# Performance work log

Measured on AMD Instinct MI355X. Metric: run time of the kernel, lower is better.

## Reference

```python
import jax, jax.numpy as jnp
import numpy as np

K = 3
TAPS = K * K
STD = float(np.sqrt(2.0)) / K  # FilterNorm scale: relu gain / kernel_size


def filter_norm(f, axis):
    # torch FilterNorm: subtract mean, divide by unbiased std (+1e-10), scale by STD
    m = jnp.mean(f, axis=axis, keepdims=True)
    sd = jnp.std(f, axis=axis, keepdims=True, ddof=1)
    return (f - m) / (sd + 1e-10) * STD


def setup_inputs() -> dict:
    key = jax.random.key(0)
    ks = jax.random.split(key, 9)
    B, C, H, W = 4, 64, 192, 192
    mid = int(C * 0.2)  # se_ratio=0.2 -> 12
    f = lambda k, shape, s: jax.random.normal(k, shape, jnp.float32) * s
    return {
        'x':   f(ks[0], (B, C, H, W), 1.0),
        'sw':  f(ks[1], (TAPS, C), 0.05),        # spatial branch 1x1 conv weight
        'sb':  f(ks[2], (TAPS,), 0.05),
        'cw1': f(ks[3], (mid, C), 0.05),         # channel branch squeeze
        'cb1': f(ks[4], (mid,), 0.05),
        'cw2': f(ks[5], (C * TAPS, mid), 0.05),  # channel branch expand
        'cb2': f(ks[6], (C * TAPS,), 0.05),
        'w2':  f(ks[7], (C, C, 1, 9), 0.05),     # trailing 1x9 conv
        'b2':  f(ks[8], (C,), 0.05),
    }


def block_forward(x, sw, sb, cw1, cb1, cw2, cb2, w2, b2):
    B, C, H, W = x.shape
    # --- DDFPack ---
    # spatial filters: 1x1 conv -> (B, 9, H, W), FilterNorm across the 9 taps
    s = jnp.einsum('bchw,tc->bthw', x, sw) + sb[None, :, None, None]
    s = filter_norm(s, axis=1)
    # channel filters: GAP -> 1x1 -> relu -> 1x1 -> (B, C, 9), FilterNorm over taps
    g = x.mean(axis=(2, 3))                         # (B, C)
    h1 = jax.nn.relu(g @ cw1.T + cb1)               # (B, mid)
    cf = (h1 @ cw2.T + cb2).reshape(B, C, TAPS)     # (B, C, 9)
    cf = filter_norm(cf, axis=2)
    # decoupled dynamic filter apply: per-pixel depthwise 3x3, combine='mul', pad=1
    xp = jnp.pad(x, ((0, 0), (0, 0), (1, 1), (1, 1)))
    out = jnp.zeros_like(x)
    for idx in range(TAPS):  # fixed 9-tap loop, no big unfold intermediate
        i, j = idx // K, idx % K
        out = out + xp[:, :, i:i + H, j:j + W] * s[:, idx:idx + 1] * cf[:, :, idx, None, None]
    # --- LeakyReLU(0.1) -> 1x9 conv (pad (0,4)) -> residual add (res_scale=1) ---
    a = jnp.where(out >= 0, out, 0.1 * out)
    y = jax.lax.conv_general_dilated(a, w2, (1, 1), ((0, 0), (4, 4)),
                                     dimension_numbers=('NCHW', 'OIHW', 'NCHW'))
    y = y + b2[None, :, None, None]
    return x + y


def reference(x, sw, sb, cw1, cb1, cw2, cb2, w2, b2):
    return block_forward(x, sw, sb, cw1, cb1, cw2, cb2, w2, b2)
```

## Files before the change

### kernel.cpp

```cpp
#include <hip/hip_runtime.h>
#include <hip/hip_bf16.h>

#define B_    4
#define C_    64
#define H_    192
#define W_    192
#define TAPS_ 9
#define MID_  12
#define HW_   (H_ * W_)
#define K_TOT 576
#define AT_STRIDE 72

constexpr float STD_ = 0.47140452079103173f;

using bf16 = __hip_bfloat16;
typedef __attribute__((ext_vector_type(4))) float  f32x4;
typedef __attribute__((ext_vector_type(8))) short  short8;

__device__ __forceinline__ unsigned short f2bf_bits(float v) {
    union { bf16 h; unsigned short u; } cv;
    cv.h = __float2bfloat16(v);
    return cv.u;
}

__device__ __forceinline__ int at_word(int row, int cw) {
    int key = (row >> 2) & 7;
    return row * (AT_STRIDE / 2) + ((((cw >> 2) ^ key) & 7) << 2) + (cw & 3);
}

__global__ __launch_bounds__(256) void k_pre(const float* __restrict__ x,
                                             const float* __restrict__ w2,
                                             unsigned short* __restrict__ w2bf,
                                             float* __restrict__ partials) {
    int bx = blockIdx.x;
    if (bx < 144) {
        int d = bx * 256 + threadIdx.x;
        int o = d / K_TOT;
        int rem = d - o * K_TOT;
        int t = rem >> 6;
        int c = rem & 63;
        w2bf[d] = f2bf_bits(w2[(o * C_ + c) * TAPS_ + t]);
        return;
    }
    bx -= 144;
    int bc = bx / 3, part = bx - 3 * (bx / 3);
    const float4* p = (const float4*)(x + (size_t)bc * HW_ + part * 12288);
    float s = 0.f;
    #pragma unroll
    for (int k = 0; k < 12; ++k) {
        float4 u = p[threadIdx.x + k * 256];
        s += u.x + u.y + u.z + u.w;
    }
    #pragma unroll
    for (int off = 32; off; off >>= 1) s += __shfl_down(s, off);
    __shared__ float red[4];
    if ((threadIdx.x & 63) == 0) red[threadIdx.x >> 6] = s;
    __syncthreads();
    if (threadIdx.x == 0)
        partials[bx] = red[0] + red[1] + red[2] + red[3];
}

__global__ __launch_bounds__(256, 3) void k_main(const float* __restrict__ x,
                                                 const float* __restrict__ sw,
                                                 const float* __restrict__ sb,
                                                 const float* __restrict__ partials,
                                                 const float* __restrict__ cw1,
                                                 const float* __restrict__ cb1,
                                                 const float* __restrict__ cw2,
                                                 const float* __restrict__ cb2,
                                                 const unsigned short* __restrict__ w2bf,
                                                 const float* __restrict__ bias2,
                                                 float* __restrict__ out) {
    __shared__ __align__(16) char smem[38624];
    short*          aT    = (short*)smem;
    unsigned*       aT32  = (unsigned*)smem;
    float*          sw_l  = (float*)smem;
    float*          s_l   = (float*)(smem + 28800);
    float*          b2_l  = (float*)(smem + 35712);
    float*          sb_l  = (float*)(smem + 35968);
    float*          cfn_l = (float*)(smem + 36016);
    float*          h1_l  = (float*)(smem + 38320);
    float*          g_l   = (float*)(smem + 38368);

    int bx = blockIdx.x;
    int bh = (bx & 7) * 96 + (bx >> 3);
    int bb = bh / H_;
    int h  = bh - bb * H_;
    int tid = threadIdx.x;
    int lane = tid & 63, wid = tid >> 6;
    int quad = lane >> 4, l16 = lane & 15;
    int obase = wid * 16;

    for (int i = tid; i < TAPS_ * C_; i += 256) sw_l[i] = sw[i];
    if (tid < C_) b2_l[tid] = bias2[tid];
    if (tid < TAPS_) sb_l[tid] = sb[tid];
    __syncthreads();

    const short* w2s = (const short*)w2bf;
    const short* arow = w2s + (obase + l16) * K_TOT + quad * 8;
    short8 a0 = *(const short8*)(arow);
    short8 a1 = *(const short8*)(arow + 32);

    if (tid < W_) {
        int w = tid;
        float acc[TAPS_];
        #pragma unroll
        for (int t = 0; t < TAPS_; ++t) acc[t] = sb_l[t];
        const float* px = x + (size_t)bb * C_ * HW_ + h * W_ + w;
        #pragma unroll 16
        for (int c = 0; c < C_; ++c) {
            float xv = px[(size_t)c * HW_];
            #pragma unroll
            for (int t = 0; t < TAPS_; ++t) acc[t] = fmaf(xv, sw_l[t * C_ + c], acc[t]);
        }
        float mean = 0.f;
        #pragma unroll
        for (int t = 0; t < TAPS_; ++t) mean += acc[t];
        mean *= (1.f / TAPS_);
        float var = 0.f;
        #pragma unroll
        for (int t = 0; t < TAPS_; ++t) { float d = acc[t] - mean; var += d * d; }
        var *= (1.f / (TAPS_ - 1));
        float scale = STD_ / (sqrtf(fmaxf(var, 0.f)) + 1e-10f);
        float* sp = s_l + (w & 3) * 432 + (w >> 2);
        #pragma unroll
        for (int t = 0; t < TAPS_; ++t) sp[t * 48] = (acc[t] - mean) * scale;
    } else {
        int c = lane;
        const float* pp = partials + (bb * C_ + c) * 3;
        g_l[c] = (pp[0] + pp[1] + pp[2]) * (1.0f / HW_);
        if (c < MID_) {
            float acc = cb1[c];
            #pragma unroll 8
            for (int cc = 0; cc < C_; ++cc) acc += g_l[cc] * cw1[c * C_ + cc];
            h1_l[c] = fmaxf(acc, 0.f);
        }
        float f[TAPS_];
        float mean = 0.f;
        #pragma unroll
        for (int t = 0; t < TAPS_; ++t) {
            int n = c * TAPS_ + t;
            float acc = cb2[n];
            #pragma unroll
            for (int m = 0; m < MID_; ++m) acc += h1_l[m] * cw2[n * MID_ + m];
            f[t] = acc;
            mean += acc;
        }
        mean *= (1.f / TAPS_);
        float var = 0.f;
        #pragma unroll
        for (int t = 0; t < TAPS_; ++t) { float d = f[t] - mean; var += d * d; }
        var *= (1.f / (TAPS_ - 1));
        float scale = STD_ / (sqrtf(fmaxf(var, 0.f)) + 1e-10f);
        #pragma unroll
        for (int t = 0; t < TAPS_; ++t)
            cfn_l[c * TAPS_ + t] = (f[t] - mean) * scale;
    }
    __syncthreads();

    for (int i = tid; i < 8 * (AT_STRIDE / 2); i += 256) {
        int rowIdx = i / (AT_STRIDE / 2);
        int col    = i - rowIdx * (AT_STRIDE / 2);
        int r = (rowIdx < 4) ? rowIdx : (192 + rowIdx);
        aT32[r * (AT_STRIDE / 2) + col] = 0u;
    }

    {
        int wbase = wid * 16;
        if (lane < 48) {
            int w0 = 4 * lane;
            float sreg[4][TAPS_];
            #pragma unroll
            for (int k = 0; k < 4; ++k) {
                const float* sp = s_l + k * 432 + lane;
                #pragma unroll
                for (int t = 0; t < TAPS_; ++t) sreg[k][t] = sp[t * 48];
            }
            bool l0 = (lane == 0), l47 = (lane == 47);
            int rok0 = (h > 0), rok2 = (h < H_ - 1);
            const float* xbase = x + (long)bb * C_ * HW_ + (long)(h - 1) * W_;
            #pragma unroll 2
            for (int i = 0; i < 16; i += 2) {
                int c0 = wbase + i;
                int cu = __builtin_amdgcn_readfirstlane(c0);
                const float* cfp = cfn_l + cu * TAPS_;
                const float* pc0 = xbase + (long)c0 * HW_;
                const float* pc1 = pc0 + HW_;
                float acc0[4] = {0.f, 0.f, 0.f, 0.f};
                float acc1[4] = {0.f, 0.f, 0.f, 0.f};
                #pragma unroll
                for (int r = 0; r < 3; ++r) {
                    if (r == 0 && !rok0) continue;
                    if (r == 2 && !rok2) continue;
                    const float* p0 = pc0 + r * W_;
                    const float* p1 = pc1 + r * W_;
                    float4 fa = *(const float4*)(p0 + w0);
                    float4 fb = *(const float4*)(p1 + w0);
                    float ma = __shfl_up(fa.w, 1);   ma = l0  ? 0.f : ma;
                    float mb = __shfl_up(fb.w, 1);   mb = l0  ? 0.f : mb;
                    float pa = __shfl_down(fa.x, 1); pa = l47 ? 0.f : pa;
                    float pb = __shfl_down(fb.x, 1); pb = l47 ? 0.f : pb;
                    float va[6] = { ma, fa.x, fa.y, fa.z, fa.w, pa };
                    float vb[6] = { mb, fb.x, fb.y, fb.z, fb.w, pb };
                    #pragma unroll
                    for (int dc = 0; dc < 3; ++dc) {
                        int t = r * 3 + dc;
                        float cva = cfp[t];
                        float cvb = cfp[TAPS_ + t];
                        #pragma unroll
                        for (int k = 0; k < 4; ++k) {
                            acc0[k] = fmaf(va[k + dc] * sreg[k][t], cva, acc0[k]);
                            acc1[k] = fmaf(vb[k + dc] * sreg[k][t], cvb, acc1[k]);
                        }
                    }
                }
                int cw = c0 >> 1;
                #pragma unroll
                for (int k = 0; k < 4; ++k) {
                    float a0v = acc0[k]; a0v = (a0v >= 0.f) ? a0v : 0.1f * a0v;
                    float a1v = acc1[k]; a1v = (a1v >= 0.f) ? a1v : 0.1f * a1v;
                    unsigned pk = (unsigned)f2bf_bits(a0v)
                                | ((unsigned)f2bf_bits(a1v) << 16);
                    aT32[at_word(w0 + k + 4, cw)] = pk;
                }
            }
        }
    }
    __syncthreads();

    {
        f32x4 acc[12];
        #pragma unroll
        for (int n = 0; n < 12; ++n) acc[n] = (f32x4){0.f, 0.f, 0.f, 0.f};

        #pragma unroll 1
        for (int kk = 0; kk < 18; ++kk) {
            short8 a2 = a1;
            if (kk < 16) a2 = *(const short8*)(arow + (kk + 2) * 32);
            int t = kk >> 1;
            int ch = ((kk & 1) << 2) + quad;
            int rowb = l16 + t;
            int key0 = (rowb >> 2) & 7;
            int off0 = rowb * AT_STRIDE + (((ch ^ key0) & 7) << 3);
            int off1 = rowb * AT_STRIDE + (((ch ^ key0 ^ 4) & 7) << 3);
            #pragma unroll
            for (int n = 0; n < 12; ++n) {
                int off = ((n & 1) ? off1 : off0) + n * 16 * AT_STRIDE;
                short8 bf = *(const short8*)(aT + off);
                acc[n] = __builtin_amdgcn_mfma_f32_16x16x32_bf16(a0, bf, acc[n], 0, 0, 0);
            }
            a0 = a1; a1 = a2;
        }

        size_t xbase = (size_t)bb * C_ * HW_ + (size_t)h * W_;
        #pragma unroll
        for (int n = 0; n < 12; ++n) {
            int w = n * 16 + l16;
            #pragma unroll
            for (int reg = 0; reg < 4; ++reg) {
                int o = obase + quad * 4 + reg;
                size_t idx = xbase + (size_t)o * HW_ + w;
                out[idx] = acc[n][reg] + b2_l[o] + x[idx];
            }
        }
    }
}

extern "C" void kernel_launch(void* const* d_in, const int* in_sizes, int n_in,
                              void* d_out, int out_size, void* d_ws, size_t ws_size,
                              hipStream_t stream) {
    const float* x   = (const float*)d_in[0];
    const float* sw  = (const float*)d_in[1];
    const float* sb  = (const float*)d_in[2];
    const float* cw1 = (const float*)d_in[3];
    const float* cb1 = (const float*)d_in[4];
    const float* cw2 = (const float*)d_in[5];
    const float* cb2 = (const float*)d_in[6];
    const float* w2  = (const float*)d_in[7];
    const float* b2  = (const float*)d_in[8];
    float* out = (float*)d_out;

    unsigned short* w2bf = (unsigned short*)d_ws;
    float* partials = (float*)((char*)d_ws + 73728);

    hipLaunchKernelGGL(k_pre, dim3(912), dim3(256), 0, stream, x, w2, w2bf, partials);
    hipLaunchKernelGGL(k_main, dim3(B_ * H_), dim3(256), 0, stream,
                       x, sw, sb, partials, cw1, cb1, cw2, cb2, w2bf, b2, out);
}
```

Before: 145.4 us.

## Prefetch input rows and batch channel loads to hide global memory latency

The spatial-filter 1x1 conv now issues its channel loads in batches of 16 into registers, with sched_barriers separating load and FMA groups, so many loads are in flight before the math starts. The dynamic-filter apply loop now software-pipelines its three input rows per channel pair: the first pair is loaded before the spatial phase and the next pair is prefetched during each iteration. Boundary rows are clamped and then zeroed by multiplying with a flag instead of branching. This aims to overlap global memory latency with compute, at the cost of higher register pressure and possible occupancy loss.

```diff
diff --git a/kernel.cpp b/kernel.cpp
--- a/kernel.cpp
+++ b/kernel.cpp
@@ -90,6 +90,7 @@
     int lane = tid & 63, wid = tid >> 6;
     int quad = lane >> 4, l16 = lane & 15;
     int obase = wid * 16;
+    int w0 = 4 * lane;
 
     for (int i = tid; i < TAPS_ * C_; i += 256) sw_l[i] = sw[i];
     if (tid < C_) b2_l[tid] = bias2[tid];
@@ -101,18 +102,61 @@
     short8 a0 = *(const short8*)(arow);
     short8 a1 = *(const short8*)(arow + 32);
 
+    long ro0 = (long)((h > 0) ? (h - 1) : h) * W_;
+    long ro1 = (long)h * W_;
+    long ro2 = (long)((h < H_ - 1) ? (h + 1) : h) * W_;
+    const float* xc = x + (size_t)bb * C_ * HW_;
+
+    float4 P0a, P1a, P2a, P0b, P1b, P2b;
+    if (lane < 48) {
+        const float* q0 = xc + (size_t)(wid * 16) * HW_;
+        const float* q1 = q0 + HW_;
+        P0a = *(const float4*)(q0 + ro0 + w0);
+        P1a = *(const float4*)(q0 + ro1 + w0);
+        P2a = *(const float4*)(q0 + ro2 + w0);
+        P0b = *(const float4*)(q1 + ro0 + w0);
+        P1b = *(const float4*)(q1 + ro1 + w0);
+        P2b = *(const float4*)(q1 + ro2 + w0);
+    }
+
     if (tid < W_) {
         int w = tid;
         float acc[TAPS_];
         #pragma unroll
         for (int t = 0; t < TAPS_; ++t) acc[t] = sb_l[t];
         const float* px = x + (size_t)bb * C_ * HW_ + h * W_ + w;
-        #pragma unroll 16
-        for (int c = 0; c < C_; ++c) {
-            float xv = px[(size_t)c * HW_];
-            #pragma unroll
-            for (int t = 0; t < TAPS_; ++t) acc[t] = fmaf(xv, sw_l[t * C_ + c], acc[t]);
-        }
+        float xv0[16], xv1[16];
+        #pragma unroll
+        for (int j = 0; j < 16; ++j) xv0[j] = px[(size_t)j * HW_];
+        #pragma unroll
+        for (int j = 0; j < 16; ++j) xv1[j] = px[(size_t)(16 + j) * HW_];
+        __builtin_amdgcn_sched_barrier(0);
+        #pragma unroll
+        for (int j = 0; j < 16; ++j)
+            #pragma unroll
+            for (int t = 0; t < TAPS_; ++t)
+                acc[t] = fmaf(xv0[j], sw_l[t * C_ + j], acc[t]);
+        #pragma unroll
+        for (int j = 0; j < 16; ++j) xv0[j] = px[(size_t)(32 + j) * HW_];
+        __builtin_amdgcn_sched_barrier(0);
+        #pragma unroll
+        for (int j = 0; j < 16; ++j)
+            #pragma unroll
+            for (int t = 0; t < TAPS_; ++t)
+                acc[t] = fmaf(xv1[j], sw_l[t * C_ + 16 + j], acc[t]);
+        #pragma unroll
+        for (int j = 0; j < 16; ++j) xv1[j] = px[(size_t)(48 + j) * HW_];
+        __builtin_amdgcn_sched_barrier(0);
+        #pragma unroll
+        for (int j = 0; j < 16; ++j)
+            #pragma unroll
+            for (int t = 0; t < TAPS_; ++t)
+                acc[t] = fmaf(xv0[j], sw_l[t * C_ + 32 + j], acc[t]);
+        #pragma unroll
+        for (int j = 0; j < 16; ++j)
+            #pragma unroll
+            for (int t = 0; t < TAPS_; ++t)
+                acc[t] = fmaf(xv1[j], sw_l[t * C_ + 48 + j], acc[t]);
         float mean = 0.f;
         #pragma unroll
         for (int t = 0; t < TAPS_; ++t) mean += acc[t];
@@ -166,9 +210,7 @@
     }
 
     {
-        int wbase = wid * 16;
         if (lane < 48) {
-            int w0 = 4 * lane;
             float sreg[4][TAPS_];
             #pragma unroll
             for (int k = 0; k < 4; ++k) {
@@ -177,43 +219,57 @@
                 for (int t = 0; t < TAPS_; ++t) sreg[k][t] = sp[t * 48];
             }
             bool l0 = (lane == 0), l47 = (lane == 47);
-            int rok0 = (h > 0), rok2 = (h < H_ - 1);
-            const float* xbase = x + (long)bb * C_ * HW_ + (long)(h - 1) * W_;
-            #pragma unroll 2
+            float rok0f = (h > 0)      ? 1.f : 0.f;
+            float rok2f = (h < H_ - 1) ? 1.f : 0.f;
+
+#define TAPROW(RR, FA, FB)                                                     \
+            do {                                                               \
+                float ma = __shfl_up(FA.w, 1);   ma = l0  ? 0.f : ma;          \
+                float mb = __shfl_up(FB.w, 1);   mb = l0  ? 0.f : mb;          \
+                float pa = __shfl_down(FA.x, 1); pa = l47 ? 0.f : pa;          \
+                float pb = __shfl_down(FB.x, 1); pb = l47 ? 0.f : pb;          \
+                float va[6] = { ma, FA.x, FA.y, FA.z, FA.w, pa };              \
+                float vb[6] = { mb, FB.x, FB.y, FB.z, FB.w, pb };              \
+                _Pragma("unroll")                                              \
+                for (int dc = 0; dc < 3; ++dc) {                               \
+                    int t = (RR) * 3 + dc;                                     \
+                    float cva = cfp[t];                                        \
+                    float cvb = cfp[TAPS_ + t];                                \
+                    _Pragma("unroll")                                          \
+                    for (int k = 0; k < 4; ++k) {                              \
+                        acc0[k] = fmaf(va[k + dc] * sreg[k][t], cva, acc0[k]); \
+                        acc1[k] = fmaf(vb[k + dc] * sreg[k][t], cvb, acc1[k]); \
+                    }                                                          \
+                }                                                              \
+            } while (0)
+
+            #pragma unroll 1
             for (int i = 0; i < 16; i += 2) {
-                int c0 = wbase + i;
+                int c0 = wid * 16 + i;
                 int cu = __builtin_amdgcn_readfirstlane(c0);
                 const float* cfp = cfn_l + cu * TAPS_;
-                const float* pc0 = xbase + (long)c0 * HW_;
-                const float* pc1 = pc0 + HW_;
+                float4 C0a = P0a, C1a = P1a, C2a = P2a;
+                float4 C0b = P0b, C1b = P1b, C2b = P2b;
+                if (i < 14) {
+                    const float* q0 = xc + (size_t)(c0 + 2) * HW_;
+                    const float* q1 = q0 + HW_;
+                    P0a = *(const float4*)(q0 + ro0 + w0);
+                    P1a = *(const float4*)(q0 + ro1 + w0);
+                    P2a = *(const float4*)(q0 + ro2 + w0);
+                    P0b = *(const float4*)(q1 + ro0 + w0);
+                    P1b = *(const float4*)(q1 + ro1 + w0);
+                    P2b = *(const float4*)(q1 + ro2 + w0);
+                }
+                __builtin_amdgcn_sched_barrier(0);
+                C0a.x *= rok0f; C0a.y *= rok0f; C0a.z *= rok0f; C0a.w *= rok0f;
+                C0b.x *= rok0f; C0b.y *= rok0f; C0b.z *= rok0f; C0b.w *= rok0f;
+                C2a.x *= rok2f; C2a.y *= rok2f; C2a.z *= rok2f; C2a.w *= rok2f;
+                C2b.x *= rok2f; C2b.y *= rok2f; C2b.z *= rok2f; C2b.w *= rok2f;
                 float acc0[4] = {0.f, 0.f, 0.f, 0.f};
                 float acc1[4] = {0.f, 0.f, 0.f, 0.f};
-                #pragma unroll
-                for (int r = 0; r < 3; ++r) {
-                    if (r == 0 && !rok0) continue;
-                    if (r == 2 && !rok2) continue;
-                    const float* p0 = pc0 + r * W_;
-                    const float* p1 = pc1 + r * W_;
-                    float4 fa = *(const float4*)(p0 + w0);
-                    float4 fb = *(const float4*)(p1 + w0);
-                    float ma = __shfl_up(fa.w, 1);   ma = l0  ? 0.f : ma;
-                    float mb = __shfl_up(fb.w, 1);   mb = l0  ? 0.f : mb;
-                    float pa = __shfl_down(fa.x, 1); pa = l47 ? 0.f : pa;
-                    float pb = __shfl_down(fb.x, 1); pb = l47 ? 0.f : pb;
-                    float va[6] = { ma, fa.x, fa.y, fa.z, fa.w, pa };
-                    float vb[6] = { mb, fb.x, fb.y, fb.z, fb.w, pb };
-                    #pragma unroll
-                    for (int dc = 0; dc < 3; ++dc) {
-                        int t = r * 3 + dc;
-                        float cva = cfp[t];
-                        float cvb = cfp[TAPS_ + t];
-                        #pragma unroll
-                        for (int k = 0; k < 4; ++k) {
-                            acc0[k] = fmaf(va[k + dc] * sreg[k][t], cva, acc0[k]);
-                            acc1[k] = fmaf(vb[k + dc] * sreg[k][t], cvb, acc1[k]);
-                        }
-                    }
-                }
+                TAPROW(0, C0a, C0b);
+                TAPROW(1, C1a, C1b);
+                TAPROW(2, C2a, C2b);
                 int cw = c0 >> 1;
                 #pragma unroll
                 for (int k = 0; k < 4; ++k) {
@@ -224,6 +280,7 @@
                     aT32[at_word(w0 + k + 4, cw)] = pk;
                 }
             }
+#undef TAPROW
         }
     }
     __syncthreads();
```

Result: faster. 138.5 us (-4.8%).
